# Performance work log

Measured on AMD Instinct MI355X. Metric: run time of the kernel, lower is better.

The kernel has to match this reference:

```python
import jax, jax.numpy as jnp
import numpy as np
import math

B, S, D, H = 4, 1024, 1024, 16
F = 4 * D
DK = D // H

def layer_norm(x, g, b, eps=1e-5):
    mu = jnp.mean(x, axis=-1, keepdims=True)
    var = jnp.var(x, axis=-1, keepdims=True)
    return (x - mu) * jax.lax.rsqrt(var + eps) * g + b

def setup_inputs() -> dict:
    key = jax.random.key(0)
    ks = jax.random.split(key, 8)
    s = 0.02
    return {
        "x": jax.random.normal(ks[0], (B, S, D), dtype=jnp.float32),
        "Wq": jax.random.normal(ks[1], (D, D), dtype=jnp.float32) * s,
        "Wk": jax.random.normal(ks[2], (D, D), dtype=jnp.float32) * s,
        "Wv": jax.random.normal(ks[3], (D, D), dtype=jnp.float32) * s,
        "Wo": jax.random.normal(ks[4], (D, D), dtype=jnp.float32) * s,
        "w1": jax.random.normal(ks[5], (F, D), dtype=jnp.float32) * s,
        "b1": jnp.zeros((F,), dtype=jnp.float32),
        "w2": jax.random.normal(ks[6], (D, F), dtype=jnp.float32) * s,
        "b2": jnp.zeros((D,), dtype=jnp.float32),
        "ln1_g": jnp.ones((D,), dtype=jnp.float32),
        "ln1_b": jnp.zeros((D,), dtype=jnp.float32),
        "ln2_g": jnp.ones((D,), dtype=jnp.float32),
        "ln2_b": jnp.zeros((D,), dtype=jnp.float32),
        "mask": jnp.ones((B, S, S), dtype=jnp.int32),
    }

def reference(x, Wq, Wk, Wv, Wo, w1, b1, w2, b2, ln1_g, ln1_b, ln2_g, ln2_b, mask):
    # --- attention sublayer (pre-norm residual) ---
    h = layer_norm(x, ln1_g, ln1_b)
    def split_heads(t):  # [B,S,D] -> [B,H,S,DK]
        return t.reshape(B, S, H, DK).transpose(0, 2, 1, 3)
    q = split_heads(h @ Wq.T)
    k = split_heads(h @ Wk.T)
    v = split_heads(h @ Wv.T)
    scores = jnp.einsum('bhqd,bhkd->bhqk', q, k) / math.sqrt(DK)
    m = (mask[:, None, :, :] != 0)  # [B,1,S,S] broadcast over heads
    scores = jnp.where(m, scores, -1e9)
    p = jax.nn.softmax(scores, axis=-1)
    p = jnp.where(m, p, 0.0)
    ctx = jnp.einsum('bhqk,bhkd->bhqd', p, v)
    ctx = ctx.transpose(0, 2, 1, 3).reshape(B, S, D)
    x = x + ctx @ Wo.T
    # --- FFN sublayer (pre-norm residual) ---
    h2 = layer_norm(x, ln2_g, ln2_b)
    y = jax.nn.gelu(h2 @ w1.T + b1, approximate=False) @ w2.T + b2
    row_valid = jnp.sum(mask, axis=-1) > 0  # [B,S]
    y = jnp.where(row_valid[..., None], y, 0.0)
    return x + y
```

## Files before the change

kernel.cpp:

```cpp
#include <hip/hip_runtime.h>

typedef unsigned short u16;
typedef unsigned int   u32;
typedef unsigned long long u64;

typedef __bf16 bf16_t;
typedef bf16_t bf16x8 __attribute__((ext_vector_type(8)));
typedef float  f32x4  __attribute__((ext_vector_type(4)));

static constexpr int Bz = 4, Sq = 1024, Dm = 1024, Hn = 16, Ff = 4096, Mtok = 4096;
static constexpr int QS = 3072;

static __device__ __forceinline__ u16 f2bf(float f) {
  u32 u = __builtin_bit_cast(u32, f);
  u32 r = u + 0x7fff + ((u >> 16) & 1);
  return (u16)(r >> 16);
}

static __device__ __forceinline__ void gld16(const u16* g, u16* l) {
  __builtin_amdgcn_global_load_lds((const __attribute__((address_space(1))) u32*)g,
                                   (__attribute__((address_space(3))) u32*)l, 16, 0, 0);
}

__global__ void k_cvt(const float* __restrict__ src, u16* __restrict__ dst, int n4) {
  int i = blockIdx.x * 256 + threadIdx.x;
  if (i >= n4) return;
  float4 v = reinterpret_cast<const float4*>(src)[i];
  ushort4 o;
  o.x = f2bf(v.x); o.y = f2bf(v.y); o.z = f2bf(v.z); o.w = f2bf(v.w);
  reinterpret_cast<ushort4*>(dst)[i] = o;
}

__global__ void k_maskpack(const int* __restrict__ mask, u32* __restrict__ mb,
                           u32* __restrict__ rv) {
  int row = blockIdx.x;
  int t = threadIdx.x, w = t >> 6, lane = t & 63;
  const int* mrow = mask + (size_t)row * Sq;
  __shared__ u32 red[4];
  u32 any = 0;
#pragma unroll
  for (int i = 0; i < 4; i++) {
    int chunk = w * 4 + i;
    int k = chunk * 64 + lane;
    u64 bal = __ballot(mrow[k] != 0);
    any |= (u32)(bal | (bal >> 32));
    if (lane == 0) mb[(size_t)row * 32 + chunk * 2]     = (u32)bal;
    if (lane == 1) mb[(size_t)row * 32 + chunk * 2 + 1] = (u32)(bal >> 32);
  }
  if (lane == 0) red[w] = any;
  __syncthreads();
  if (t == 0) rv[row] = (red[0] | red[1] | red[2] | red[3]) ? 1u : 0u;
}

__global__ void k_ln(const float* __restrict__ x, const float* __restrict__ g,
                     const float* __restrict__ bb, u16* __restrict__ out) {
  int row = blockIdx.x, t = threadIdx.x;
  float4 v = reinterpret_cast<const float4*>(x + (size_t)row * Dm)[t];
  float s  = v.x + v.y + v.z + v.w;
  float s2 = v.x * v.x + v.y * v.y + v.z * v.z + v.w * v.w;
#pragma unroll
  for (int m = 1; m < 64; m <<= 1) { s += __shfl_xor(s, m); s2 += __shfl_xor(s2, m); }
  __shared__ float rs[4], rs2[4];
  int w = t >> 6;
  if ((t & 63) == 0) { rs[w] = s; rs2[w] = s2; }
  __syncthreads();
  s  = rs[0] + rs[1] + rs[2] + rs[3];
  s2 = rs2[0] + rs2[1] + rs2[2] + rs2[3];
  float mu  = s * (1.0f / Dm);
  float var = s2 * (1.0f / Dm) - mu * mu;
  float r = rsqrtf(var + 1e-5f);
  float4 gv = reinterpret_cast<const float4*>(g)[t];
  float4 bv = reinterpret_cast<const float4*>(bb)[t];
  ushort4 o;
  o.x = f2bf((v.x - mu) * r * gv.x + bv.x);
  o.y = f2bf((v.y - mu) * r * gv.y + bv.y);
  o.z = f2bf((v.z - mu) * r * gv.z + bv.z);
  o.w = f2bf((v.w - mu) * r * gv.w + bv.w);
  reinterpret_cast<ushort4*>(out + (size_t)row * Dm)[t] = o;
}

template <int MODE>
__global__ __launch_bounds__(256)
void k_gemm(const u16* __restrict__ A, const u16* __restrict__ Bw,
            int M, int N, int K,
            const float* __restrict__ bias, void* __restrict__ Cout,
            u16* __restrict__ vTout) {
  __shared__ u16 As[128 * 64];
  __shared__ u16 Bs[128 * 64];
  const int t = threadIdx.x;
  const int lane = t & 63, w = t >> 6;
  const int wr = w >> 1, wc = w & 1;
  const int m0 = blockIdx.y * 128, n0 = blockIdx.x * 128;
  const int lr = lane & 15, lk = (lane >> 4) * 8;

  f32x4 acc[4][4] = {};

  for (int kt = 0; kt < K; kt += 64) {
#pragma unroll
    for (int i = 0; i < 4; i++) {
      int cc = i * 256 + t; int row = cc >> 3, c8 = cc & 7;
      gld16(A + (size_t)(m0 + row) * K + kt + c8 * 8, &As[cc * 8]);
    }
#pragma unroll
    for (int i = 0; i < 4; i++) {
      int cc = i * 256 + t; int row = cc >> 3, c8 = cc & 7;
      gld16(Bw + (size_t)(n0 + row) * K + kt + c8 * 8, &Bs[cc * 8]);
    }
    __syncthreads();
#pragma unroll
    for (int kk = 0; kk < 2; kk++) {
      bf16x8 af[4], bfg[4];
#pragma unroll
      for (int m = 0; m < 4; m++)
        af[m] = *reinterpret_cast<const bf16x8*>(&As[(wr * 64 + m * 16 + lr) * 64 + kk * 32 + lk]);
#pragma unroll
      for (int n = 0; n < 4; n++)
        bfg[n] = *reinterpret_cast<const bf16x8*>(&Bs[(wc * 64 + n * 16 + lr) * 64 + kk * 32 + lk]);
#pragma unroll
      for (int m = 0; m < 4; m++)
#pragma unroll
        for (int n = 0; n < 4; n++)
          acc[m][n] = __builtin_amdgcn_mfma_f32_16x16x32_bf16(af[m], bfg[n], acc[m][n], 0, 0, 0);
    }
    __syncthreads();
  }

  if constexpr (MODE == 0) {
    if (n0 >= 2048) {
#pragma unroll
      for (int m = 0; m < 4; m++) {
        const int rowb = m0 + wr * 64 + m * 16 + (lane >> 4) * 4;
        const int bb = rowb >> 10, tok = rowb & 1023;
#pragma unroll
        for (int n = 0; n < 4; n++) {
          const int dfull = n0 + wc * 64 + n * 16 + lr - 2048;
          ushort4 o4;
          o4.x = f2bf(acc[m][n][0]); o4.y = f2bf(acc[m][n][1]);
          o4.z = f2bf(acc[m][n][2]); o4.w = f2bf(acc[m][n][3]);
          size_t idx = ((size_t)((bb * 16 + (dfull >> 6)) * 64 + (dfull & 63))) * 1024 + tok;
          *reinterpret_cast<ushort4*>(vTout + idx) = o4;
        }
      }
      return;
    }
  }

#pragma unroll
  for (int m = 0; m < 4; m++) {
    const int rowb = m0 + wr * 64 + m * 16 + (lane >> 4) * 4;
#pragma unroll
    for (int n = 0; n < 4; n++) {
      const int col = n0 + wc * 64 + n * 16 + lr;
#pragma unroll
      for (int r = 0; r < 4; r++) {
        const int row = rowb + r;
        float v = acc[m][n][r];
        size_t idx = (size_t)row * N + col;
        if constexpr (MODE == 0) {
          ((u16*)Cout)[idx] = f2bf(v);
        } else {
          float xx = v + bias[col];
          float gl = 0.5f * xx * (1.0f + erff(xx * 0.70710678118f));
          ((u16*)Cout)[idx] = f2bf(gl);
        }
      }
    }
  }
}

template <int MODE>
__global__ __launch_bounds__(256)
void k_gemm64(const u16* __restrict__ A, const u16* __restrict__ Bw,
              int M, int N, int K,
              const float* __restrict__ resid, const float* __restrict__ bias,
              const u32* __restrict__ rv, float* __restrict__ Cout) {
  __shared__ u16 As[128 * 64];
  __shared__ u16 Bs[64 * 64];
  const int t = threadIdx.x;
  const int lane = t & 63, w = t >> 6;
  const int m0 = blockIdx.y * 128, n0 = blockIdx.x * 64;
  const int lr = lane & 15, lk = (lane >> 4) * 8;

  f32x4 acc[2][4] = {};

  for (int kt = 0; kt < K; kt += 64) {
#pragma unroll
    for (int i = 0; i < 4; i++) {
      int cc = i * 256 + t; int row = cc >> 3, c8 = cc & 7;
      gld16(A + (size_t)(m0 + row) * K + kt + c8 * 8, &As[cc * 8]);
    }
#pragma unroll
    for (int i = 0; i < 2; i++) {
      int cc = i * 256 + t; int row = cc >> 3, c8 = cc & 7;
      gld16(Bw + (size_t)(n0 + row) * K + kt + c8 * 8, &Bs[cc * 8]);
    }
    __syncthreads();
#pragma unroll
    for (int kk = 0; kk < 2; kk++) {
      bf16x8 af[2], bfg[4];
#pragma unroll
      for (int m = 0; m < 2; m++)
        af[m] = *reinterpret_cast<const bf16x8*>(&As[(w * 32 + m * 16 + lr) * 64 + kk * 32 + lk]);
#pragma unroll
      for (int n = 0; n < 4; n++)
        bfg[n] = *reinterpret_cast<const bf16x8*>(&Bs[(n * 16 + lr) * 64 + kk * 32 + lk]);
#pragma unroll
      for (int m = 0; m < 2; m++)
#pragma unroll
        for (int n = 0; n < 4; n++)
          acc[m][n] = __builtin_amdgcn_mfma_f32_16x16x32_bf16(af[m], bfg[n], acc[m][n], 0, 0, 0);
    }
    __syncthreads();
  }

#pragma unroll
  for (int m = 0; m < 2; m++) {
    const int rowb = m0 + w * 32 + m * 16 + (lane >> 4) * 4;
#pragma unroll
    for (int n = 0; n < 4; n++) {
      const int col = n0 + n * 16 + lr;
#pragma unroll
      for (int r = 0; r < 4; r++) {
        const int row = rowb + r;
        float v = acc[m][n][r];
        size_t idx = (size_t)row * N + col;
        if constexpr (MODE == 1) {
          Cout[idx] = resid[idx] + v;
        } else {
          float y = rv[row] ? (v + bias[col]) : 0.0f;
          Cout[idx] = resid[idx] + y;
        }
      }
    }
  }
}

__global__ __launch_bounds__(256)
void k_attn(const u16* __restrict__ qkv, const u16* __restrict__ vT,
            const u32* __restrict__ mb, u16* __restrict__ ctxb) {
  __shared__ u16 Qs[4096];
  __shared__ u16 Ks0[4096];
  __shared__ u16 Vt0[4096];
  __shared__ u16 Vt1[4096];
  __shared__ u16 Ps[4096];
  const int t = threadIdx.x, lane = t & 63, w = t >> 6;
  const int q0 = blockIdx.x * 64;
  const int bh = blockIdx.y, b = bh >> 4, h = bh & 15;
  const int lr = lane & 15, lkq = (lane >> 4) * 8;

  const size_t qbase = (size_t)(b * Sq + q0) * QS + h * 64;
  const size_t kbase = (size_t)(b * Sq) * QS + 1024 + h * 64;
  const size_t vbase = (size_t)bh * 64 * 1024;

  auto stageK = [&](u16* dst, int kt) {
#pragma unroll
    for (int j = 0; j < 2; j++) {
      int cc = j * 256 + t, r = cc >> 3, ch = cc & 7;
      gld16(qkv + kbase + (size_t)(kt * 64 + r) * QS + ((ch ^ (r & 7)) * 8), dst + cc * 8);
    }
  };
  auto stageV = [&](u16* dst, int kt) {
#pragma unroll
    for (int j = 0; j < 2; j++) {
      int cc = j * 256 + t, d = cc >> 3, ch = cc & 7;
      gld16(vT + vbase + (size_t)d * 1024 + kt * 64 + ((ch ^ (d & 7)) * 8), dst + cc * 8);
    }
  };

  {
#pragma unroll
    for (int j = 0; j < 2; j++) {
      int cc = j * 256 + t, r = cc >> 3, ch = cc & 7;
      gld16(qkv + qbase + (size_t)r * QS + ((ch ^ (r & 7)) * 8), &Qs[cc * 8]);
    }
  }
  stageK(Ks0, 0);
  stageV(Vt0, 0);
  __syncthreads();

  bf16x8 qf[2];
  const int qrow = w * 16 + lr;
#pragma unroll
  for (int kk = 0; kk < 2; kk++)
    qf[kk] = *reinterpret_cast<const bf16x8*>(&Qs[qrow * 64 + ((kk * 32 + lkq) ^ ((qrow & 7) << 3))]);
  __syncthreads();

  float m_i[4] = {-1e30f, -1e30f, -1e30f, -1e30f};
  float l_i[4] = {0.f, 0.f, 0.f, 0.f};
  f32x4 accO[4] = {};
  const int rq0 = (lane >> 4) * 4;

  for (int kt = 0; kt < Sq / 64; kt++) {
    u16* kb = (kt & 1) ? Qs : Ks0;
    u16* vb = (kt & 1) ? Vt1 : Vt0;
    if (kt + 1 < Sq / 64) {
      stageK((kt & 1) ? Ks0 : Qs, kt + 1);
      stageV((kt & 1) ? Vt0 : Vt1, kt + 1);
    }
    u32 mw0[4], mw1[4];
#pragma unroll
    for (int r = 0; r < 4; r++) {
      int q = q0 + w * 16 + rq0 + r;
      mw0[r] = mb[(size_t)(b * Sq + q) * 32 + kt * 2];
      mw1[r] = mb[(size_t)(b * Sq + q) * 32 + kt * 2 + 1];
    }

    f32x4 sc[4];
#pragma unroll
    for (int n = 0; n < 4; n++) sc[n] = (f32x4){0.f, 0.f, 0.f, 0.f};
#pragma unroll
    for (int kk = 0; kk < 2; kk++) {
#pragma unroll
      for (int n = 0; n < 4; n++) {
        int krow = n * 16 + lr;
        bf16x8 kf = *reinterpret_cast<const bf16x8*>(
            &kb[krow * 64 + ((kk * 32 + lkq) ^ ((krow & 7) << 3))]);
        sc[n] = __builtin_amdgcn_mfma_f32_16x16x32_bf16(qf[kk], kf, sc[n], 0, 0, 0);
      }
    }

    float rmax[4] = {-1e30f, -1e30f, -1e30f, -1e30f};
#pragma unroll
    for (int r = 0; r < 4; r++) {
      if ((mw0[r] & mw1[r]) == 0xffffffffu) {
#pragma unroll
        for (int n = 0; n < 4; n++) {
          float sval = sc[n][r] * 0.125f;
          sc[n][r] = sval;
          rmax[r] = fmaxf(rmax[r], sval);
        }
      } else {
#pragma unroll
        for (int n = 0; n < 4; n++) {
          int kin = n * 16 + lr;
          float sval = sc[n][r] * 0.125f;
          u32 word = (kin & 32) ? mw1[r] : mw0[r];
          if (!((word >> (kin & 31)) & 1)) sval = -1e9f;
          sc[n][r] = sval;
          rmax[r] = fmaxf(rmax[r], sval);
        }
      }
    }
#pragma unroll
    for (int r = 0; r < 4; r++) {
#pragma unroll
      for (int mm = 1; mm < 16; mm <<= 1) rmax[r] = fmaxf(rmax[r], __shfl_xor(rmax[r], mm));
      float mnew = fmaxf(m_i[r], rmax[r]);
      if (mnew - m_i[r] > 8.0f) {
        float scale = __expf(m_i[r] - mnew);
        m_i[r] = mnew;
        l_i[r] *= scale;
#pragma unroll
        for (int n = 0; n < 4; n++) accO[n][r] *= scale;
      }
    }
    float rsum[4] = {0.f, 0.f, 0.f, 0.f};
#pragma unroll
    for (int n = 0; n < 4; n++)
#pragma unroll
      for (int r = 0; r < 4; r++) {
        float p = __expf(sc[n][r] - m_i[r]);
        sc[n][r] = p;
        rsum[r] += p;
      }
#pragma unroll
    for (int r = 0; r < 4; r++) {
#pragma unroll
      for (int mm = 1; mm < 16; mm <<= 1) rsum[r] += __shfl_xor(rsum[r], mm);
      l_i[r] += rsum[r];
    }
#pragma unroll
    for (int n = 0; n < 4; n++)
#pragma unroll
      for (int r = 0; r < 4; r++) {
        int row = rq0 + r;
        Ps[w * 1024 + row * 64 + ((n * 16 + lr) ^ ((row & 7) << 3))] = f2bf(sc[n][r]);
      }
    asm volatile("s_waitcnt lgkmcnt(0)" ::: "memory");
    __builtin_amdgcn_sched_barrier(0);
    bf16x8 pf[2];
#pragma unroll
    for (int kk = 0; kk < 2; kk++)
      pf[kk] = *reinterpret_cast<const bf16x8*>(
          &Ps[w * 1024 + lr * 64 + ((kk * 32 + lkq) ^ ((lr & 7) << 3))]);
#pragma unroll
    for (int kk = 0; kk < 2; kk++) {
#pragma unroll
      for (int n = 0; n < 4; n++) {
        int d = n * 16 + lr;
        bf16x8 vf = *reinterpret_cast<const bf16x8*>(
            &vb[d * 64 + ((kk * 32 + lkq) ^ ((d & 7) << 3))]);
        accO[n] = __builtin_amdgcn_mfma_f32_16x16x32_bf16(pf[kk], vf, accO[n], 0, 0, 0);
      }
    }
    __syncthreads();
  }

#pragma unroll
  for (int r = 0; r < 4; r++) {
    float recip = (m_i[r] <= -0.9e9f || l_i[r] == 0.f) ? 0.f : 1.f / l_i[r];
    int grow = q0 + w * 16 + rq0 + r;
#pragma unroll
    for (int n = 0; n < 4; n++)
      ctxb[(size_t)(b * Sq + grow) * Dm + h * 64 + n * 16 + lr] = f2bf(accO[n][r] * recip);
  }
}

extern "C" void kernel_launch(void* const* d_in, const int* in_sizes, int n_in,
                              void* d_out, int out_size, void* d_ws, size_t ws_size,
                              hipStream_t stream) {
  const float* x     = (const float*)d_in[0];
  const float* Wq    = (const float*)d_in[1];
  const float* Wk    = (const float*)d_in[2];
  const float* Wv    = (const float*)d_in[3];
  const float* Wo    = (const float*)d_in[4];
  const float* w1    = (const float*)d_in[5];
  const float* b1    = (const float*)d_in[6];
  const float* w2    = (const float*)d_in[7];
  const float* b2    = (const float*)d_in[8];
  const float* ln1g  = (const float*)d_in[9];
  const float* ln1b  = (const float*)d_in[10];
  const float* ln2g  = (const float*)d_in[11];
  const float* ln2b  = (const float*)d_in[12];
  const int*   mask  = (const int*)d_in[13];
  float* out = (float*)d_out;

  char* ws = (char*)d_ws;
  const size_t MB = 1024 * 1024;
  u16* wqkv_b = (u16*)(ws + 0 * MB);
  u16* wo_b   = (u16*)(ws + 13 * MB / 2);
  u16* w1_b   = (u16*)(ws + 17 * MB / 2);
  u16* w2_b   = (u16*)(ws + 17 * MB);
  u16* h_b    = (u16*)(ws + 51 * MB / 2);
  u32* mbits  = (u32*)(ws + 34 * MB);
  u32* rv     = (u32*)(ws + 34 * MB + 600 * 1024);
  u16* qkv    = (u16*)(ws + 35 * MB);
  u16* ctxb   = (u16*)(ws + 121 * MB / 2);
  u16* vTb    = (u16*)(ws + 69 * MB);
  u16* a1b    = (u16*)(ws + 35 * MB);
  float* x1   = out;

  k_cvt<<<1024, 256, 0, stream>>>(Wq, wqkv_b,               262144);
  k_cvt<<<1024, 256, 0, stream>>>(Wk, wqkv_b + 1024 * 1024, 262144);
  k_cvt<<<1024, 256, 0, stream>>>(Wv, wqkv_b + 2048 * 1024, 262144);
  k_cvt<<<1024, 256, 0, stream>>>(Wo, wo_b, 262144);
  k_cvt<<<4096, 256, 0, stream>>>(w1, w1_b, 1048576);
  k_cvt<<<4096, 256, 0, stream>>>(w2, w2_b, 1048576);
  k_maskpack<<<4096, 256, 0, stream>>>(mask, mbits, rv);
  k_ln<<<4096, 256, 0, stream>>>(x, ln1g, ln1b, h_b);

  dim3 gqkv(QS / 128, Mtok / 128);
  k_gemm<0><<<gqkv, 256, 0, stream>>>(h_b, wqkv_b, Mtok, QS, Dm, nullptr, qkv, vTb);

  dim3 ga(Sq / 64, Bz * Hn);
  k_attn<<<ga, 256, 0, stream>>>(qkv, vTb, mbits, ctxb);

  dim3 gwo(Dm / 64, Mtok / 128);
  k_gemm64<1><<<gwo, 256, 0, stream>>>(ctxb, wo_b, Mtok, Dm, Dm, x, nullptr, nullptr, x1);

  k_ln<<<4096, 256, 0, stream>>>(x1, ln2g, ln2b, h_b);

  dim3 g2(Ff / 128, Mtok / 128);
  k_gemm<2><<<g2, 256, 0, stream>>>(h_b, w1_b, Mtok, Ff, Dm, b1, a1b, nullptr);

  dim3 gw2(Dm / 64, Mtok / 128);
  k_gemm64<3><<<gw2, 256, 0, stream>>>(a1b, w2_b, Mtok, Dm, Ff, x1, b2, rv, out);
}
```

Before: 454.1 us.

## Shrink output-projection GEMM tiles with XCD swizzle and separate V transpose kernel

The N=1024 GEMMs (Wo and w2) now use 64x64 tiles with a K-step of 128 and a block-index swizzle that groups neighbouring tiles, doubling the grid so more CUs are busy. The scattered transposed-V store in the QKV GEMM epilogue is removed and replaced by a dedicated LDS-based transpose kernel. This trades fewer FLOPs per byte of LDS traffic, plus an extra launch and an extra read and write of V, for better occupancy and coalesced stores.

```diff
diff --git a/kernel.cpp b/kernel.cpp
--- a/kernel.cpp
+++ b/kernel.cpp
@@ -83,8 +83,7 @@
 __global__ __launch_bounds__(256)
 void k_gemm(const u16* __restrict__ A, const u16* __restrict__ Bw,
             int M, int N, int K,
-            const float* __restrict__ bias, void* __restrict__ Cout,
-            u16* __restrict__ vTout) {
+            const float* __restrict__ bias, void* __restrict__ Cout) {
   __shared__ u16 As[128 * 64];
   __shared__ u16 Bs[128 * 64];
   const int t = threadIdx.x;
@@ -123,26 +122,6 @@
           acc[m][n] = __builtin_amdgcn_mfma_f32_16x16x32_bf16(af[m], bfg[n], acc[m][n], 0, 0, 0);
     }
     __syncthreads();
-  }
-
-  if constexpr (MODE == 0) {
-    if (n0 >= 2048) {
-#pragma unroll
-      for (int m = 0; m < 4; m++) {
-        const int rowb = m0 + wr * 64 + m * 16 + (lane >> 4) * 4;
-        const int bb = rowb >> 10, tok = rowb & 1023;
-#pragma unroll
-        for (int n = 0; n < 4; n++) {
-          const int dfull = n0 + wc * 64 + n * 16 + lr - 2048;
-          ushort4 o4;
-          o4.x = f2bf(acc[m][n][0]); o4.y = f2bf(acc[m][n][1]);
-          o4.z = f2bf(acc[m][n][2]); o4.w = f2bf(acc[m][n][3]);
-          size_t idx = ((size_t)((bb * 16 + (dfull >> 6)) * 64 + (dfull & 63))) * 1024 + tok;
-          *reinterpret_cast<ushort4*>(vTout + idx) = o4;
-        }
-      }
-      return;
-    }
   }
 
 #pragma unroll
@@ -174,64 +153,84 @@
               int M, int N, int K,
               const float* __restrict__ resid, const float* __restrict__ bias,
               const u32* __restrict__ rv, float* __restrict__ Cout) {
-  __shared__ u16 As[128 * 64];
-  __shared__ u16 Bs[64 * 64];
+  __shared__ u16 As[64 * 128];
+  __shared__ u16 Bs[64 * 128];
   const int t = threadIdx.x;
   const int lane = t & 63, w = t >> 6;
-  const int m0 = blockIdx.y * 128, n0 = blockIdx.x * 64;
+  const int nx = gridDim.x;
+  const int nwg = nx * gridDim.y;
+  const int bid = blockIdx.y * nx + blockIdx.x;
+  const int swz = (bid & 7) * (nwg >> 3) + (bid >> 3);
+  const int n0 = (swz % nx) * 64, m0 = (swz / nx) * 64;
   const int lr = lane & 15, lk = (lane >> 4) * 8;
 
-  f32x4 acc[2][4] = {};
-
-  for (int kt = 0; kt < K; kt += 64) {
+  f32x4 acc[4] = {};
+
+  for (int kt = 0; kt < K; kt += 128) {
 #pragma unroll
     for (int i = 0; i < 4; i++) {
-      int cc = i * 256 + t; int row = cc >> 3, c8 = cc & 7;
+      int cc = i * 256 + t; int row = cc >> 4, c8 = cc & 15;
       gld16(A + (size_t)(m0 + row) * K + kt + c8 * 8, &As[cc * 8]);
     }
 #pragma unroll
-    for (int i = 0; i < 2; i++) {
-      int cc = i * 256 + t; int row = cc >> 3, c8 = cc & 7;
+    for (int i = 0; i < 4; i++) {
+      int cc = i * 256 + t; int row = cc >> 4, c8 = cc & 15;
       gld16(Bw + (size_t)(n0 + row) * K + kt + c8 * 8, &Bs[cc * 8]);
     }
     __syncthreads();
 #pragma unroll
-    for (int kk = 0; kk < 2; kk++) {
-      bf16x8 af[2], bfg[4];
-#pragma unroll
-      for (int m = 0; m < 2; m++)
-        af[m] = *reinterpret_cast<const bf16x8*>(&As[(w * 32 + m * 16 + lr) * 64 + kk * 32 + lk]);
-#pragma unroll
-      for (int n = 0; n < 4; n++)
-        bfg[n] = *reinterpret_cast<const bf16x8*>(&Bs[(n * 16 + lr) * 64 + kk * 32 + lk]);
-#pragma unroll
-      for (int m = 0; m < 2; m++)
-#pragma unroll
-        for (int n = 0; n < 4; n++)
-          acc[m][n] = __builtin_amdgcn_mfma_f32_16x16x32_bf16(af[m], bfg[n], acc[m][n], 0, 0, 0);
+    for (int kk = 0; kk < 4; kk++) {
+      bf16x8 af = *reinterpret_cast<const bf16x8*>(&As[(w * 16 + lr) * 128 + kk * 32 + lk]);
+#pragma unroll
+      for (int n = 0; n < 4; n++) {
+        bf16x8 bfg = *reinterpret_cast<const bf16x8*>(&Bs[(n * 16 + lr) * 128 + kk * 32 + lk]);
+        acc[n] = __builtin_amdgcn_mfma_f32_16x16x32_bf16(af, bfg, acc[n], 0, 0, 0);
+      }
     }
     __syncthreads();
   }
 
-#pragma unroll
-  for (int m = 0; m < 2; m++) {
-    const int rowb = m0 + w * 32 + m * 16 + (lane >> 4) * 4;
-#pragma unroll
-    for (int n = 0; n < 4; n++) {
-      const int col = n0 + n * 16 + lr;
-#pragma unroll
-      for (int r = 0; r < 4; r++) {
-        const int row = rowb + r;
-        float v = acc[m][n][r];
-        size_t idx = (size_t)row * N + col;
-        if constexpr (MODE == 1) {
-          Cout[idx] = resid[idx] + v;
-        } else {
-          float y = rv[row] ? (v + bias[col]) : 0.0f;
-          Cout[idx] = resid[idx] + y;
-        }
-      }
-    }
+  const int rowb = m0 + w * 16 + (lane >> 4) * 4;
+#pragma unroll
+  for (int n = 0; n < 4; n++) {
+    const int col = n0 + n * 16 + lr;
+#pragma unroll
+    for (int r = 0; r < 4; r++) {
+      const int row = rowb + r;
+      float v = acc[n][r];
+      size_t idx = (size_t)row * N + col;
+      if constexpr (MODE == 1) {
+        Cout[idx] = resid[idx] + v;
+      } else {
+        float y = rv[row] ? (v + bias[col]) : 0.0f;
+        Cout[idx] = resid[idx] + y;
+      }
+    }
+  }
+}
+
+__global__ __launch_bounds__(256)
+void k_vtrans(const u16* __restrict__ qkv, u16* __restrict__ vT) {
+  __shared__ u16 tile[64 * 72];
+  const int t = threadIdx.x;
+  const int tt = blockIdx.x;
+  const int bh = blockIdx.y, b = bh >> 4, h = bh & 15;
+  const u16* src = qkv + (size_t)(b * Sq + tt * 64) * QS + 2048 + h * 64;
+#pragma unroll
+  for (int j = 0; j < 2; j++) {
+    int cc = j * 256 + t, row = cc >> 3, dc0 = (cc & 7) * 8;
+    uint4 v = *reinterpret_cast<const uint4*>(src + (size_t)row * QS + dc0);
+    *reinterpret_cast<uint4*>(&tile[row * 72 + dc0]) = v;
+  }
+  __syncthreads();
+#pragma unroll
+  for (int j = 0; j < 2; j++) {
+    int cc = j * 256 + t, d = cc >> 3, tk0 = (cc & 7) * 8;
+    u16 tmp[8];
+#pragma unroll
+    for (int e = 0; e < 8; e++) tmp[e] = tile[(tk0 + e) * 72 + d];
+    *reinterpret_cast<uint4*>(vT + (size_t)bh * 65536 + (size_t)d * 1024 + tt * 64 + tk0) =
+        *reinterpret_cast<uint4*>(tmp);
   }
 }
 
@@ -250,7 +249,7 @@
 
   const size_t qbase = (size_t)(b * Sq + q0) * QS + h * 64;
   const size_t kbase = (size_t)(b * Sq) * QS + 1024 + h * 64;
-  const size_t vbase = (size_t)bh * 64 * 1024;
+  const size_t vbase = (size_t)bh * 65536;
 
   auto stageK = [&](u16* dst, int kt) {
 #pragma unroll
@@ -450,19 +449,22 @@
   k_ln<<<4096, 256, 0, stream>>>(x, ln1g, ln1b, h_b);
 
   dim3 gqkv(QS / 128, Mtok / 128);
-  k_gemm<0><<<gqkv, 256, 0, stream>>>(h_b, wqkv_b, Mtok, QS, Dm, nullptr, qkv, vTb);
+  k_gemm<0><<<gqkv, 256, 0, stream>>>(h_b, wqkv_b, Mtok, QS, Dm, nullptr, qkv);
+
+  dim3 gvt(Sq / 64, Bz * Hn);
+  k_vtrans<<<gvt, 256, 0, stream>>>(qkv, vTb);
 
   dim3 ga(Sq / 64, Bz * Hn);
   k_attn<<<ga, 256, 0, stream>>>(qkv, vTb, mbits, ctxb);
 
-  dim3 gwo(Dm / 64, Mtok / 128);
+  dim3 gwo(Dm / 64, Mtok / 64);
   k_gemm64<1><<<gwo, 256, 0, stream>>>(ctxb, wo_b, Mtok, Dm, Dm, x, nullptr, nullptr, x1);
 
   k_ln<<<4096, 256, 0, stream>>>(x1, ln2g, ln2b, h_b);
 
   dim3 g2(Ff / 128, Mtok / 128);
-  k_gemm<2><<<g2, 256, 0, stream>>>(h_b, w1_b, Mtok, Ff, Dm, b1, a1b, nullptr);
-
-  dim3 gw2(Dm / 64, Mtok / 128);
+  k_gemm<2><<<g2, 256, 0, stream>>>(h_b, w1_b, Mtok, Ff, Dm, b1, a1b);
+
+  dim3 gw2(Dm / 64, Mtok / 64);
   k_gemm64<3><<<gw2, 256, 0, stream>>>(a1b, w2_b, Mtok, Dm, Ff, x1, b2, rv, out);
 }
```

Measured after the change: 550.9 us. 1.21x slower.
